# Performance work log

Measured on AMD Instinct MI355X. Metric: run time of the kernel, lower is better.

## Reference

```python
import jax, jax.numpy as jnp
import numpy as np

CE_TEMP = 1.0
SIMW_TEMP = 0.1
NSEG = 2048
EPS = 1e-8
NEG = jnp.float32(-1e30)


def setup_inputs() -> dict:
    key = jax.random.key(0)
    k1, k2, k3, k4, k5, k6 = jax.random.split(key, 6)
    N, C, H, W, Ch, S = 2, 19, 128, 128, 256, NSEG
    inputs_plbl = jax.random.normal(k1, (N, C, H, W), dtype=jnp.float32)
    feats_plbl = jax.random.normal(k2, (N, Ch, H, W), dtype=jnp.float32)
    inputs = jax.random.normal(k3, (N, C, H, W), dtype=jnp.float32)
    # multi-hot targets per superpixel; ~2.3 active classes on average -> many multi-hot rows
    targets = jax.random.bernoulli(k4, 0.12, (N, S, C)).astype(jnp.float32)
    superpixels = jax.random.randint(k5, (N, H, W), 0, S, dtype=jnp.int32)
    spmasks = jax.random.bernoulli(k6, 0.5, (N, H, W))
    return {"inputs_plbl": inputs_plbl, "feats_plbl": feats_plbl, "inputs": inputs,
            "targets": targets, "superpixels": superpixels, "spmasks": spmasks}


def _per_image(out_plbl, feat, out, trg_table, sp, mask):
    # out_plbl: [HW,C] softmax'd pseudo-label probs; feat: [HW,Ch]; out: [HW,C];
    # trg_table: [S,C] multi-hot; sp: [HW] int superpixel ids; mask: [HW] bool
    HW, C = out_plbl.shape
    S = trg_table.shape[0]
    trg_pix = trg_table[sp]                                  # [HW,C]
    multi_spx = trg_table.sum(-1) > 1.0                      # [S]
    valid = mask & multi_spx[sp]                             # == spmask & multi-hot mask

    # scatter_max: argmax pixel per (superpixel, class) among valid pixels
    scores = jnp.where(valid[:, None], out_plbl, NEG)
    seg_max = jax.ops.segment_max(scores, sp, num_segments=S)       # [S,C]
    is_max = valid[:, None] & (scores >= seg_max[sp])
    cand = jnp.where(is_max, jnp.arange(HW, dtype=jnp.int32)[:, None], HW)
    proto_idx = jax.ops.segment_min(cand, sp, num_segments=S)       # [S,C]
    proto_idx = jnp.clip(proto_idx, 0, HW - 1)

    # prototype features and per-pixel similarities to own-superpixel class prototypes
    proto_feat = feat[proto_idx]                             # [S,C,Ch]
    pf_pix = proto_feat[sp]                                  # [HW,C,Ch] (dominant intermediate)
    sim = jnp.einsum('kcd,kd->kc', pf_pix, feat) / SIMW_TEMP  # [HW,C]

    # scatter_softmax over the active classes of the pixel's superpixel
    active = trg_pix > 0.0
    w_multi = jax.nn.softmax(jnp.where(active, sim, NEG), axis=-1)
    w_row = jnp.where(active, w_multi, trg_pix)              # inactive entries keep 0
    w = jnp.where(valid[:, None], w_row, trg_pix)            # non-multi pixels keep one-hot
    w = jax.lax.stop_gradient(w)                             # original computes weights under no_grad

    ce = -jnp.log(out + EPS)                                 # [HW,C]
    contrib = jnp.where(mask[:, None], w * ce, 0.0)
    any_valid = jnp.any(valid)                               # image skipped if no multi-hot masked pixel
    loss_i = jnp.where(any_valid, contrib.sum(), 0.0)
    cnt_i = jnp.where(any_valid, mask.sum(), 0)
    return loss_i, cnt_i


def reference(inputs_plbl, feats_plbl, inputs, targets, superpixels, spmasks):
    N, C, H, W = inputs_plbl.shape
    Ch = feats_plbl.shape[1]
    out_plbl = jax.nn.softmax(inputs_plbl / CE_TEMP, axis=1).transpose(0, 2, 3, 1).reshape(N, -1, C)
    feats = feats_plbl.transpose(0, 2, 3, 1).reshape(N, -1, Ch)
    out = jax.nn.softmax(inputs / CE_TEMP, axis=1).transpose(0, 2, 3, 1).reshape(N, -1, C)
    sp = superpixels.reshape(N, -1)
    mask = spmasks.reshape(N, -1)
    loss_i, cnt_i = jax.vmap(_per_image)(out_plbl, feats, out, targets, sp, mask)
    total = loss_i.sum()
    cnt = cnt_i.sum()
    return jnp.where(cnt > 0, total / jnp.maximum(cnt, 1).astype(jnp.float32), 0.0)
```

## Files before the change

### kernel.cpp

```cpp
#include <hip/hip_runtime.h>
#include <cstdint>
#include <cstddef>

#define NN   2
#define CC   19
#define HWD  16384
#define CH   256
#define SS   2048
#define BCAP 32

#define EPSV 1e-8f

__global__ void k_multi(const float* __restrict__ trg, int* __restrict__ multi,
                        int* __restrict__ sp_cnt, float* __restrict__ slots,
                        int* __restrict__ cnt, int* __restrict__ vcnt) {
    int i = blockIdx.x * blockDim.x + threadIdx.x;
    if (i >= NN * SS) return;
    const float* t = trg + (size_t)i * CC;
    float s = 0.f;
    #pragma unroll
    for (int c = 0; c < CC; ++c) s += t[c];
    multi[i] = (s > 1.0f) ? 1 : 0;
    sp_cnt[i] = 0;
    if (i < 256) slots[i] = 0.f;
    if (i < 2) { cnt[i] = 0; vcnt[i] = 0; }
}

__global__ __launch_bounds__(256) void k_main(
        const float* __restrict__ xp, const float* __restrict__ xi,
        const float* __restrict__ trg, const int* __restrict__ sp,
        const int* __restrict__ msk, const int* __restrict__ multi,
        int* __restrict__ sp_cnt, unsigned short* __restrict__ bucket,
        unsigned char* __restrict__ validf, float* __restrict__ plbl_pm,
        float* __restrict__ ce_pm, int* __restrict__ cnt,
        int* __restrict__ vcnt, float* __restrict__ slots) {
    int idx = blockIdx.x * blockDim.x + threadIdx.x;
    int n = idx >> 14;
    int k = idx & (HWD - 1);
    int lane = threadIdx.x & 63;
    int m = (msk[idx] != 0);
    int s = sp[idx];
    int mu = multi[n * SS + s];
    int valid = m && mu;
    validf[idx] = (unsigned char)valid;
    unsigned long long mb = __ballot(m);
    unsigned long long vb = __ballot(valid);

    if (valid) {
        int cell = n * SS + s;
        int pos = atomicAdd(&sp_cnt[cell], 1);
        if (pos < BCAP) bucket[(size_t)cell * BCAP + pos] = (unsigned short)k;
        const float* a = xp + (size_t)n * CC * HWD + k;
        float v[CC];
        float mx = -1e30f;
        #pragma unroll
        for (int c = 0; c < CC; ++c) { v[c] = a[(size_t)c * HWD]; mx = fmaxf(mx, v[c]); }
        float su = 0.f;
        #pragma unroll
        for (int c = 0; c < CC; ++c) { v[c] = expf(v[c] - mx); su += v[c]; }
        float inv = 1.f / su;
        float* op = plbl_pm + (size_t)idx * CC;
        #pragma unroll
        for (int c = 0; c < CC; ++c) op[c] = v[c] * inv;
    }

    float contrib = 0.f;
    if (m) {
        const float* b = xi + (size_t)n * CC * HWD + k;
        float v[CC];
        float mx = -1e30f;
        #pragma unroll
        for (int c = 0; c < CC; ++c) { v[c] = b[(size_t)c * HWD]; mx = fmaxf(mx, v[c]); }
        float su = 0.f;
        #pragma unroll
        for (int c = 0; c < CC; ++c) { v[c] = expf(v[c] - mx); su += v[c]; }
        float inv = 1.f / su;
        if (mu) {
            float* cp = ce_pm + (size_t)idx * CC;
            #pragma unroll
            for (int c = 0; c < CC; ++c) cp[c] = -logf(v[c] * inv + EPSV);
        } else {
            const float* t = trg + ((size_t)n * SS + s) * CC;
            #pragma unroll
            for (int c = 0; c < CC; ++c) contrib += t[c] * (-logf(v[c] * inv + EPSV));
        }
    }
    #pragma unroll
    for (int off = 32; off >= 1; off >>= 1) contrib += __shfl_xor(contrib, off);
    if (lane == 0) {
        if (mb) atomicAdd(&cnt[n], __popcll(mb));
        if (vb) atomicAdd(&vcnt[n], __popcll(vb));
        if (contrib != 0.f) atomicAdd(&slots[n * 128 + ((idx >> 6) & 127)], contrib);
    }
}

__global__ void k_transpose(const float* __restrict__ F,
                            const unsigned char* __restrict__ validf,
                            float* __restrict__ FT) {
    __shared__ float tile[64][65];
    __shared__ unsigned char vld[64];
    int n  = blockIdx.z;
    int k0 = blockIdx.x * 64;
    int d0 = blockIdx.y * 64;
    const float* src = F + (size_t)n * CH * HWD;
    float* dst = FT + (size_t)n * HWD * CH;
    int tx = threadIdx.x, ty = threadIdx.y;
    if (ty == 0) vld[tx] = validf[n * HWD + k0 + tx];
    #pragma unroll
    for (int i = 0; i < 16; ++i) {
        int dd = ty + 4 * i;
        tile[dd][tx] = src[(size_t)(d0 + dd) * HWD + (k0 + tx)];
    }
    __syncthreads();
    #pragma unroll
    for (int i = 0; i < 16; ++i) {
        int kk = ty + 4 * i;
        if (vld[kk]) dst[(size_t)(k0 + kk) * CH + (d0 + tx)] = tile[tx][kk];
    }
}

__global__ __launch_bounds__(256) void k_sim(
        const float* __restrict__ feat_t, const float* __restrict__ ce_pm,
        const float* __restrict__ plbl_pm, const float* __restrict__ trg,
        const int* __restrict__ sp_cnt, const unsigned short* __restrict__ bucket,
        const int* __restrict__ multi, float* __restrict__ slots) {
    int id = blockIdx.x;
    if (!multi[id]) return;
    int cnt = sp_cnt[id];
    if (cnt == 0) return;
    cnt = min(cnt, BCAP);
    int n    = id >> 11;
    int tid  = threadIdx.x;
    int lane = tid & 63;
    int wv   = tid >> 6;

    __shared__ float protoF[CC][CH];
    __shared__ int   s_proto[CC];
    __shared__ int   actc[CC];

    float t = (lane < CC) ? trg[(size_t)id * CC + lane] : 0.f;
    unsigned long long act = __ballot(t > 0.f);
    int nact = __popcll(act);
    int apos = __popcll(act & ((1ull << lane) - 1ull));
    if ((act >> lane) & 1ull) actc[apos] = lane;
    int mypix = (lane < cnt) ? (int)bucket[(size_t)id * BCAP + lane] : 0;

    if (wv == 0) {
        float bv = -1e30f;
        int   bi = HWD;
        for (int i = 0; i < cnt; ++i) {
            int pix = __shfl(mypix, i);
            if (lane < CC) {
                float v = plbl_pm[((size_t)(n * HWD + pix)) * CC + lane];
                if (v > bv || (v == bv && pix < bi)) { bv = v; bi = pix; }
            }
        }
        if ((act >> lane) & 1ull) s_proto[apos] = bi;
    }
    __syncthreads();

    for (int a = wv; a < nact; a += 4) {
        int p = s_proto[a];
        ((float4*)(&protoF[a][0]))[lane] =
            ((const float4*)(feat_t + ((size_t)(n * HWD + p)) * CH))[lane];
    }
    __syncthreads();

    float wcontrib = 0.f;
    for (int i = wv; i < cnt; i += 4) {
        int pix = __shfl(mypix, i);
        float4 f = ((const float4*)(feat_t + ((size_t)(n * HWD + pix)) * CH))[lane];
        float mysim = -1e30f;
        for (int a = 0; a < nact; ++a) {
            float4 pf = ((const float4*)(&protoF[a][0]))[lane];
            float d = f.x * pf.x + f.y * pf.y + f.z * pf.z + f.w * pf.w;
            #pragma unroll
            for (int off = 32; off >= 1; off >>= 1) d += __shfl_xor(d, off);
            if (lane == a) mysim = d * 10.0f;
        }
        float mx = mysim;
        #pragma unroll
        for (int off = 32; off >= 1; off >>= 1) mx = fmaxf(mx, __shfl_xor(mx, off));
        float e = (lane < nact) ? expf(mysim - mx) : 0.f;
        float se = e;
        #pragma unroll
        for (int off = 32; off >= 1; off >>= 1) se += __shfl_xor(se, off);
        float ce = (lane < nact)
                 ? ce_pm[((size_t)(n * HWD + pix)) * CC + actc[lane]] : 0.f;
        float c1 = (e / se) * ce;
        #pragma unroll
        for (int off = 32; off >= 1; off >>= 1) c1 += __shfl_xor(c1, off);
        wcontrib += c1;
    }
    if (lane == 0 && wcontrib != 0.f)
        atomicAdd(&slots[n * 128 + (id & 127)], wcontrib);
}

__global__ void k_final(const float* __restrict__ slots, const int* __restrict__ cnt,
                        const int* __restrict__ vcnt, float* __restrict__ out) {
    __shared__ float red[2];
    int t = threadIdx.x;
    int w = t >> 6;
    int lane = t & 63;
    float v = slots[w * 128 + lane] + slots[w * 128 + lane + 64];
    #pragma unroll
    for (int off = 32; off >= 1; off >>= 1) v += __shfl_xor(v, off);
    if (lane == 0) red[w] = v;
    __syncthreads();
    if (t == 0) {
        float total = 0.f;
        int c = 0;
        for (int n = 0; n < NN; ++n)
            if (vcnt[n] > 0) { total += red[n]; c += cnt[n]; }
        out[0] = (c > 0) ? total / (float)c : 0.f;
    }
}

extern "C" void kernel_launch(void* const* d_in, const int* in_sizes, int n_in,
                              void* d_out, int out_size, void* d_ws, size_t ws_size,
                              hipStream_t stream) {
    const float* inputs_plbl = (const float*)d_in[0];
    const float* feats_plbl  = (const float*)d_in[1];
    const float* inputs      = (const float*)d_in[2];
    const float* targets     = (const float*)d_in[3];
    const int*   superpixels = (const int*)d_in[4];
    const int*   spmasks     = (const int*)d_in[5];
    float* out = (float*)d_out;

    char* ws = (char*)d_ws;
    int*   sp_cnt = (int*)ws;
    int*   cnt    = (int*)(ws + 16384);
    int*   vcnt   = (int*)(ws + 16392);
    float* slots  = (float*)(ws + 16416);
    unsigned char*  validf = (unsigned char*)(ws + 17440);
    unsigned short* bucket = (unsigned short*)(ws + 50208);
    int*   multi  = (int*)(ws + 312352);
    float* plbl_pm = (float*)(ws + 328736);
    float* ce_pm   = (float*)(ws + 2819104);
    float* feat_t  = (float*)(ws + 5309472);

    k_multi<<<(NN * SS + 255) / 256, 256, 0, stream>>>(targets, multi, sp_cnt,
                                                       slots, cnt, vcnt);
    k_main<<<(NN * HWD) / 256, 256, 0, stream>>>(inputs_plbl, inputs, targets,
                                                 superpixels, spmasks, multi,
                                                 sp_cnt, bucket, validf,
                                                 plbl_pm, ce_pm, cnt, vcnt, slots);
    dim3 tg(HWD / 64, CH / 64, NN);
    k_transpose<<<tg, dim3(64, 4), 0, stream>>>(feats_plbl, validf, feat_t);
    k_sim<<<NN * SS, 256, 0, stream>>>(feat_t, ce_pm, plbl_pm, targets,
                                       sp_cnt, bucket, multi, slots);
    k_final<<<1, 128, 0, stream>>>(slots, cnt, vcnt, out);
}
```

Baseline: 136.0 us.

## Fuse multi-hot and final kernels, split main kernel halves, parallelize prototype argmax

```diff
diff --git a/kernel.cpp b/kernel.cpp
--- a/kernel.cpp
+++ b/kernel.cpp
@@ -11,86 +11,82 @@
 
 #define EPSV 1e-8f
 
-__global__ void k_multi(const float* __restrict__ trg, int* __restrict__ multi,
-                        int* __restrict__ sp_cnt, float* __restrict__ slots,
-                        int* __restrict__ cnt, int* __restrict__ vcnt) {
-    int i = blockIdx.x * blockDim.x + threadIdx.x;
-    if (i >= NN * SS) return;
-    const float* t = trg + (size_t)i * CC;
-    float s = 0.f;
-    #pragma unroll
-    for (int c = 0; c < CC; ++c) s += t[c];
-    multi[i] = (s > 1.0f) ? 1 : 0;
-    sp_cnt[i] = 0;
-    if (i < 256) slots[i] = 0.f;
-    if (i < 2) { cnt[i] = 0; vcnt[i] = 0; }
-}
-
 __global__ __launch_bounds__(256) void k_main(
         const float* __restrict__ xp, const float* __restrict__ xi,
         const float* __restrict__ trg, const int* __restrict__ sp,
-        const int* __restrict__ msk, const int* __restrict__ multi,
+        const int* __restrict__ msk,
         int* __restrict__ sp_cnt, unsigned short* __restrict__ bucket,
         unsigned char* __restrict__ validf, float* __restrict__ plbl_pm,
         float* __restrict__ ce_pm, int* __restrict__ cnt,
         int* __restrict__ vcnt, float* __restrict__ slots) {
-    int idx = blockIdx.x * blockDim.x + threadIdx.x;
+    int gid = blockIdx.x * blockDim.x + threadIdx.x;
+    int partB = (gid >= NN * HWD);
+    int idx = partB ? gid - NN * HWD : gid;
     int n = idx >> 14;
     int k = idx & (HWD - 1);
     int lane = threadIdx.x & 63;
     int m = (msk[idx] != 0);
     int s = sp[idx];
-    int mu = multi[n * SS + s];
+    const float* t = trg + ((size_t)n * SS + s) * CC;
+    int mu = 0;
+    if (m) {
+        float ts = 0.f;
+        #pragma unroll
+        for (int c = 0; c < CC; ++c) ts += t[c];
+        mu = (ts > 1.0f);
+    }
     int valid = m && mu;
-    validf[idx] = (unsigned char)valid;
-    unsigned long long mb = __ballot(m);
-    unsigned long long vb = __ballot(valid);
-
-    if (valid) {
-        int cell = n * SS + s;
-        int pos = atomicAdd(&sp_cnt[cell], 1);
-        if (pos < BCAP) bucket[(size_t)cell * BCAP + pos] = (unsigned short)k;
-        const float* a = xp + (size_t)n * CC * HWD + k;
-        float v[CC];
-        float mx = -1e30f;
+
+    if (!partB) {
+        validf[idx] = (unsigned char)valid;
+        unsigned long long mb = __ballot(m);
+        unsigned long long vb = __ballot(valid);
+        if (valid) {
+            int cell = n * SS + s;
+            int pos = atomicAdd(&sp_cnt[cell], 1);
+            if (pos < BCAP) bucket[(size_t)cell * BCAP + pos] = (unsigned short)k;
+            const float* a = xp + (size_t)n * CC * HWD + k;
+            float v[CC];
+            float mx = -1e30f;
+            #pragma unroll
+            for (int c = 0; c < CC; ++c) { v[c] = a[(size_t)c * HWD]; mx = fmaxf(mx, v[c]); }
+            float su = 0.f;
+            #pragma unroll
+            for (int c = 0; c < CC; ++c) { v[c] = expf(v[c] - mx); su += v[c]; }
+            float inv = 1.f / su;
+            float* op = plbl_pm + (size_t)idx * CC;
+            #pragma unroll
+            for (int c = 0; c < CC; ++c) op[c] = v[c] * inv;
+        }
+        if (lane == 0) {
+            if (mb) atomicAdd(&cnt[n], __popcll(mb));
+            if (vb) atomicAdd(&vcnt[n], __popcll(vb));
+        }
+    } else {
+        float contrib = 0.f;
+        if (m) {
+            const float* b = xi + (size_t)n * CC * HWD + k;
+            float v[CC];
+            float mx = -1e30f;
+            #pragma unroll
+            for (int c = 0; c < CC; ++c) { v[c] = b[(size_t)c * HWD]; mx = fmaxf(mx, v[c]); }
+            float su = 0.f;
+            #pragma unroll
+            for (int c = 0; c < CC; ++c) { v[c] = expf(v[c] - mx); su += v[c]; }
+            float inv = 1.f / su;
+            if (mu) {
+                float* cp = ce_pm + (size_t)idx * CC;
+                #pragma unroll
+                for (int c = 0; c < CC; ++c) cp[c] = -logf(v[c] * inv + EPSV);
+            } else {
+                #pragma unroll
+                for (int c = 0; c < CC; ++c) contrib += t[c] * (-logf(v[c] * inv + EPSV));
+            }
+        }
         #pragma unroll
-        for (int c = 0; c < CC; ++c) { v[c] = a[(size_t)c * HWD]; mx = fmaxf(mx, v[c]); }
-        float su = 0.f;
-        #pragma unroll
-        for (int c = 0; c < CC; ++c) { v[c] = expf(v[c] - mx); su += v[c]; }
-        float inv = 1.f / su;
-        float* op = plbl_pm + (size_t)idx * CC;
-        #pragma unroll
-        for (int c = 0; c < CC; ++c) op[c] = v[c] * inv;
-    }
-
-    float contrib = 0.f;
-    if (m) {
-        const float* b = xi + (size_t)n * CC * HWD + k;
-        float v[CC];
-        float mx = -1e30f;
-        #pragma unroll
-        for (int c = 0; c < CC; ++c) { v[c] = b[(size_t)c * HWD]; mx = fmaxf(mx, v[c]); }
-        float su = 0.f;
-        #pragma unroll
-        for (int c = 0; c < CC; ++c) { v[c] = expf(v[c] - mx); su += v[c]; }
-        float inv = 1.f / su;
-        if (mu) {
-            float* cp = ce_pm + (size_t)idx * CC;
-            #pragma unroll
-            for (int c = 0; c < CC; ++c) cp[c] = -logf(v[c] * inv + EPSV);
-        } else {
-            const float* t = trg + ((size_t)n * SS + s) * CC;
-            #pragma unroll
-            for (int c = 0; c < CC; ++c) contrib += t[c] * (-logf(v[c] * inv + EPSV));
-        }
-    }
-    #pragma unroll
-    for (int off = 32; off >= 1; off >>= 1) contrib += __shfl_xor(contrib, off);
-    if (lane == 0) {
-        if (mb) atomicAdd(&cnt[n], __popcll(mb));
-        if (vb) atomicAdd(&vcnt[n], __popcll(vb));
-        if (contrib != 0.f) atomicAdd(&slots[n * 128 + ((idx >> 6) & 127)], contrib);
+        for (int off = 32; off >= 1; off >>= 1) contrib += __shfl_xor(contrib, off);
+        if (lane == 0 && contrib != 0.f)
+            atomicAdd(&slots[n * 128 + ((idx >> 6) & 127)], contrib);
     }
 }
 
@@ -123,96 +119,116 @@
         const float* __restrict__ feat_t, const float* __restrict__ ce_pm,
         const float* __restrict__ plbl_pm, const float* __restrict__ trg,
         const int* __restrict__ sp_cnt, const unsigned short* __restrict__ bucket,
-        const int* __restrict__ multi, float* __restrict__ slots) {
-    int id = blockIdx.x;
-    if (!multi[id]) return;
-    int cnt = sp_cnt[id];
-    if (cnt == 0) return;
-    cnt = min(cnt, BCAP);
-    int n    = id >> 11;
+        float* __restrict__ slots, const int* __restrict__ cnt,
+        const int* __restrict__ vcnt, int* __restrict__ done,
+        float* __restrict__ out) {
+    int id   = blockIdx.x;
     int tid  = threadIdx.x;
     int lane = tid & 63;
     int wv   = tid >> 6;
+    int cnt_c = sp_cnt[id];
 
     __shared__ float protoF[CC][CH];
+    __shared__ float s_bv[4][CC];
+    __shared__ int   s_bi[4][CC];
     __shared__ int   s_proto[CC];
     __shared__ int   actc[CC];
 
-    float t = (lane < CC) ? trg[(size_t)id * CC + lane] : 0.f;
-    unsigned long long act = __ballot(t > 0.f);
-    int nact = __popcll(act);
-    int apos = __popcll(act & ((1ull << lane) - 1ull));
-    if ((act >> lane) & 1ull) actc[apos] = lane;
-    int mypix = (lane < cnt) ? (int)bucket[(size_t)id * BCAP + lane] : 0;
-
-    if (wv == 0) {
+    if (cnt_c > 0) {
+        cnt_c = min(cnt_c, BCAP);
+        int n = id >> 11;
+        float t = (lane < CC) ? trg[(size_t)id * CC + lane] : 0.f;
+        unsigned long long act = __ballot(t > 0.f);
+        int nact = __popcll(act);
+        int apos = __popcll(act & ((1ull << lane) - 1ull));
+        if ((act >> lane) & 1ull) actc[apos] = lane;
+        int mypix = (lane < cnt_c) ? (int)bucket[(size_t)id * BCAP + lane] : 0;
+
         float bv = -1e30f;
         int   bi = HWD;
-        for (int i = 0; i < cnt; ++i) {
+        for (int i = wv; i < cnt_c; i += 4) {
             int pix = __shfl(mypix, i);
             if (lane < CC) {
                 float v = plbl_pm[((size_t)(n * HWD + pix)) * CC + lane];
                 if (v > bv || (v == bv && pix < bi)) { bv = v; bi = pix; }
             }
         }
-        if ((act >> lane) & 1ull) s_proto[apos] = bi;
+        if (lane < CC) { s_bv[wv][lane] = bv; s_bi[wv][lane] = bi; }
+        __syncthreads();
+        if (lane < CC) {
+            bv = -1e30f; bi = HWD;
+            #pragma unroll
+            for (int j = 0; j < 4; ++j) {
+                float v = s_bv[j][lane];
+                int   p = s_bi[j][lane];
+                if (v > bv || (v == bv && p < bi)) { bv = v; bi = p; }
+            }
+            if ((act >> lane) & 1ull) s_proto[apos] = bi;
+        }
+        __syncthreads();
+
+        for (int a = wv; a < nact; a += 4) {
+            int p = s_proto[a];
+            ((float4*)(&protoF[a][0]))[lane] =
+                ((const float4*)(feat_t + ((size_t)(n * HWD + p)) * CH))[lane];
+        }
+        __syncthreads();
+
+        float wcontrib = 0.f;
+        for (int i = wv; i < cnt_c; i += 4) {
+            int pix = __shfl(mypix, i);
+            float ce = (lane < nact)
+                     ? ce_pm[((size_t)(n * HWD + pix)) * CC + actc[lane]] : 0.f;
+            float4 f = ((const float4*)(feat_t + ((size_t)(n * HWD + pix)) * CH))[lane];
+            float mysim = -1e30f;
+            for (int a = 0; a < nact; ++a) {
+                float4 pf = ((const float4*)(&protoF[a][0]))[lane];
+                float d = f.x * pf.x + f.y * pf.y + f.z * pf.z + f.w * pf.w;
+                #pragma unroll
+                for (int off = 32; off >= 1; off >>= 1) d += __shfl_xor(d, off);
+                if (lane == a) mysim = d * 10.0f;
+            }
+            float mx = mysim;
+            #pragma unroll
+            for (int off = 32; off >= 1; off >>= 1) mx = fmaxf(mx, __shfl_xor(mx, off));
+            float e = (lane < nact) ? expf(mysim - mx) : 0.f;
+            float se = e;
+            #pragma unroll
+            for (int off = 32; off >= 1; off >>= 1) se += __shfl_xor(se, off);
+            float c1 = (e / se) * ce;
+            #pragma unroll
+            for (int off = 32; off >= 1; off >>= 1) c1 += __shfl_xor(c1, off);
+            wcontrib += c1;
+        }
+        if (lane == 0 && wcontrib != 0.f)
+            atomicAdd(&slots[n * 128 + (id & 127)], wcontrib);
     }
     __syncthreads();
 
-    for (int a = wv; a < nact; a += 4) {
-        int p = s_proto[a];
-        ((float4*)(&protoF[a][0]))[lane] =
-            ((const float4*)(feat_t + ((size_t)(n * HWD + p)) * CH))[lane];
-    }
-    __syncthreads();
-
-    float wcontrib = 0.f;
-    for (int i = wv; i < cnt; i += 4) {
-        int pix = __shfl(mypix, i);
-        float4 f = ((const float4*)(feat_t + ((size_t)(n * HWD + pix)) * CH))[lane];
-        float mysim = -1e30f;
-        for (int a = 0; a < nact; ++a) {
-            float4 pf = ((const float4*)(&protoF[a][0]))[lane];
-            float d = f.x * pf.x + f.y * pf.y + f.z * pf.z + f.w * pf.w;
-            #pragma unroll
-            for (int off = 32; off >= 1; off >>= 1) d += __shfl_xor(d, off);
-            if (lane == a) mysim = d * 10.0f;
-        }
-        float mx = mysim;
-        #pragma unroll
-        for (int off = 32; off >= 1; off >>= 1) mx = fmaxf(mx, __shfl_xor(mx, off));
-        float e = (lane < nact) ? expf(mysim - mx) : 0.f;
-        float se = e;
-        #pragma unroll
-        for (int off = 32; off >= 1; off >>= 1) se += __shfl_xor(se, off);
-        float ce = (lane < nact)
-                 ? ce_pm[((size_t)(n * HWD + pix)) * CC + actc[lane]] : 0.f;
-        float c1 = (e / se) * ce;
-        #pragma unroll
-        for (int off = 32; off >= 1; off >>= 1) c1 += __shfl_xor(c1, off);
-        wcontrib += c1;
-    }
-    if (lane == 0 && wcontrib != 0.f)
-        atomicAdd(&slots[n * 128 + (id & 127)], wcontrib);
-}
-
-__global__ void k_final(const float* __restrict__ slots, const int* __restrict__ cnt,
-                        const int* __restrict__ vcnt, float* __restrict__ out) {
-    __shared__ float red[2];
-    int t = threadIdx.x;
-    int w = t >> 6;
-    int lane = t & 63;
-    float v = slots[w * 128 + lane] + slots[w * 128 + lane + 64];
-    #pragma unroll
-    for (int off = 32; off >= 1; off >>= 1) v += __shfl_xor(v, off);
-    if (lane == 0) red[w] = v;
-    __syncthreads();
-    if (t == 0) {
-        float total = 0.f;
-        int c = 0;
-        for (int n = 0; n < NN; ++n)
-            if (vcnt[n] > 0) { total += red[n]; c += cnt[n]; }
-        out[0] = (c > 0) ? total / (float)c : 0.f;
+    if (wv == 0) {
+        int old = 0;
+        __threadfence();
+        if (lane == 0) old = atomicAdd(done, 1);
+        old = __shfl(old, 0);
+        if (old == (int)gridDim.x - 1) {
+            __threadfence();
+            float v0 = atomicAdd(&slots[lane], 0.f)
+                     + atomicAdd(&slots[64 + lane], 0.f);
+            float v1 = atomicAdd(&slots[128 + lane], 0.f)
+                     + atomicAdd(&slots[192 + lane], 0.f);
+            #pragma unroll
+            for (int off = 32; off >= 1; off >>= 1) {
+                v0 += __shfl_xor(v0, off);
+                v1 += __shfl_xor(v1, off);
+            }
+            if (lane == 0) {
+                float total = 0.f;
+                int c = 0;
+                if (vcnt[0] > 0) { total += v0; c += cnt[0]; }
+                if (vcnt[1] > 0) { total += v1; c += cnt[1]; }
+                out[0] = (c > 0) ? total / (float)c : 0.f;
+            }
+        }
     }
 }
 
@@ -231,23 +247,22 @@
     int*   sp_cnt = (int*)ws;
     int*   cnt    = (int*)(ws + 16384);
     int*   vcnt   = (int*)(ws + 16392);
+    int*   done   = (int*)(ws + 16400);
     float* slots  = (float*)(ws + 16416);
     unsigned char*  validf = (unsigned char*)(ws + 17440);
     unsigned short* bucket = (unsigned short*)(ws + 50208);
-    int*   multi  = (int*)(ws + 312352);
-    float* plbl_pm = (float*)(ws + 328736);
-    float* ce_pm   = (float*)(ws + 2819104);
-    float* feat_t  = (float*)(ws + 5309472);
-
-    k_multi<<<(NN * SS + 255) / 256, 256, 0, stream>>>(targets, multi, sp_cnt,
-                                                       slots, cnt, vcnt);
-    k_main<<<(NN * HWD) / 256, 256, 0, stream>>>(inputs_plbl, inputs, targets,
-                                                 superpixels, spmasks, multi,
-                                                 sp_cnt, bucket, validf,
-                                                 plbl_pm, ce_pm, cnt, vcnt, slots);
+    float* plbl_pm = (float*)(ws + 312352);
+    float* ce_pm   = (float*)(ws + 2802720);
+    float* feat_t  = (float*)(ws + 5293088);
+
+    hipMemsetAsync(ws, 0, 17440, stream);
+
+    k_main<<<(2 * NN * HWD) / 256, 256, 0, stream>>>(
+        inputs_plbl, inputs, targets, superpixels, spmasks,
+        sp_cnt, bucket, validf, plbl_pm, ce_pm, cnt, vcnt, slots);
     dim3 tg(HWD / 64, CH / 64, NN);
     k_transpose<<<tg, dim3(64, 4), 0, stream>>>(feats_plbl, validf, feat_t);
     k_sim<<<NN * SS, 256, 0, stream>>>(feat_t, ce_pm, plbl_pm, targets,
-                                       sp_cnt, bucket, multi, slots);
-    k_final<<<1, 128, 0, stream>>>(slots, cnt, vcnt, out);
-}
+                                       sp_cnt, bucket, slots, cnt, vcnt,
+                                       done, out);
+}
```

Result: slower. 207.4 us (+52.5%).
